# Kernel tuning notes

Hardware: AMD Instinct MI355X
Metric: run time of the kernel (lower is better)

Reference implementation:

```python
import jax, jax.numpy as jnp
import numpy as np

_USER_BASIS = [(0, 1), (2, 1), (4, 1), (8, 1), (1, 1), (6, 1), (10, 1), (12, 1),
               (3, -1), (5, -1), (9, -1), (14, 1), (7, 1), (11, 1), (13, 1), (15, -1)]
_MASK_TO_IDX = {mask: idx for idx, (mask, _) in enumerate(_USER_BASIS)}


def _blade_sign_pga(mask_a, mask_b):
    sign = 1
    for bit in range(4):
        if mask_a >> bit & 1:
            lower = mask_b & ((1 << bit) - 1)
            if bin(lower).count('1') % 2 == 1:
                sign = -sign
    return sign


def _build_pga_cayley_table():
    # table[k, i, j] = coeff of basis_k in basis_i * basis_j; values in {-1,0,+1}
    table = np.zeros((16, 16, 16), dtype=np.float32)
    for i, (mask_i, sign_i) in enumerate(_USER_BASIS):
        for j, (mask_j, sign_j) in enumerate(_USER_BASIS):
            if mask_i & mask_j & 1:  # shared null e0 -> product vanishes
                continue
            result_mask = mask_i ^ mask_j
            anticomm = _blade_sign_pga(mask_i, mask_j)
            k = _MASK_TO_IDX[result_mask]
            _, sign_k = _USER_BASIS[k]
            table[k, i, j] = float(sign_i * sign_j * anticomm * sign_k)
    return table


def setup_inputs() -> dict:
    key = jax.random.key(0)
    k1, k2 = jax.random.split(key)
    shape = (4, 4096, 128, 16)
    mv_a = jax.random.normal(k1, shape, dtype=jnp.float32)
    mv_b = jax.random.normal(k2, shape, dtype=jnp.float32)
    cayley = jnp.asarray(_build_pga_cayley_table())  # (16,16,16) buffer
    return {"mv_a": mv_a, "mv_b": mv_b, "cayley": cayley}


def reference(mv_a, mv_b, cayley):
    # Geometric product C[..., k] = sum_ij A[..., i] B[..., j] cayley[k, i, j]
    return jnp.einsum('...i,...j,kij->...k', mv_a, mv_b, cayley)
```

## Files before the change

### kernel.cpp

```cpp
#include <hip/hip_runtime.h>


namespace {

typedef float f32x4 __attribute__((ext_vector_type(4)));

struct CayleyLUT {
    int idx[16][16];
    int sgn[16][16];
};

constexpr CayleyLUT make_lut() {
    CayleyLUT L{};
    constexpr int MASK[16] = {0, 2, 4, 8, 1, 6, 10, 12, 3, 5, 9, 14, 7, 11, 13, 15};
    constexpr int SIGN[16] = {1, 1, 1, 1, 1, 1, 1, 1, -1, -1, -1, 1, 1, 1, 1, -1};
    for (int i = 0; i < 16; ++i) {
        for (int j = 0; j < 16; ++j) {
            L.idx[i][j] = 0;
            L.sgn[i][j] = 0;
            if (MASK[i] & MASK[j] & 1) continue;
            const int rm = MASK[i] ^ MASK[j];
            int k = 0;
            for (int t = 0; t < 16; ++t)
                if (MASK[t] == rm) k = t;
            int s = 1;
            for (int bit = 0; bit < 4; ++bit) {
                if ((MASK[i] >> bit) & 1) {
                    int lower = MASK[j] & ((1 << bit) - 1);
                    int c = 0;
                    for (int x = lower; x; x >>= 1) c += x & 1;
                    if (c & 1) s = -s;
                }
            }
            L.idx[i][j] = k;
            L.sgn[i][j] = SIGN[i] * SIGN[j] * s * SIGN[k];
        }
    }
    return L;
}

constexpr CayleyLUT LUT = make_lut();

__device__ __forceinline__ int slot(int m, int q) {
    return m * 16 + ((q ^ ((m >> 1) & 3)) << 2);
}

__device__ __forceinline__ void gp_compute(const float* a, const float* b, float* c) {
#pragma unroll
    for (int k = 0; k < 16; ++k) c[k] = 0.0f;
#pragma unroll
    for (int i = 0; i < 16; ++i) {
#pragma unroll
        for (int j = 0; j < 16; ++j) {
            const int s = LUT.sgn[i][j];
            if (s != 0) {
                const int k = LUT.idx[i][j];
                c[k] = fmaf(s > 0 ? a[i] : -a[i], b[j], c[k]);
            }
        }
    }
}

__global__ __launch_bounds__(256) void gp_kernel(const float* __restrict__ A,
                                                 const float* __restrict__ B,
                                                 float* __restrict__ C,
                                                 long long n_mv) {
    __shared__ float sA[256 * 16];
    __shared__ float sB[256 * 16];
    const int t = threadIdx.x;
    const long long base_mv = (long long)blockIdx.x * 256;
    const bool full = (base_mv + 256 <= n_mv);
    const int mv_here = full ? 256 : (int)(n_mv - base_mv);
    const int nf4 = mv_here * 4;

    const f32x4* __restrict__ A4 = reinterpret_cast<const f32x4*>(A) + base_mv * 4;
    const f32x4* __restrict__ B4 = reinterpret_cast<const f32x4*>(B) + base_mv * 4;
    f32x4* __restrict__ C4 = reinterpret_cast<f32x4*>(C) + base_mv * 4;

    if (full) {
#pragma unroll
        for (int r = 0; r < 4; ++r) {
            const int f = t + 256 * r;
            const f32x4 va = A4[f];
            const f32x4 vb = B4[f];
            const int o = slot(f >> 2, f & 3);
            *reinterpret_cast<f32x4*>(&sA[o]) = va;
            *reinterpret_cast<f32x4*>(&sB[o]) = vb;
        }
    } else {
#pragma unroll
        for (int r = 0; r < 4; ++r) {
            const int f = t + 256 * r;
            if (f < nf4) {
                const f32x4 va = A4[f];
                const f32x4 vb = B4[f];
                const int o = slot(f >> 2, f & 3);
                *reinterpret_cast<f32x4*>(&sA[o]) = va;
                *reinterpret_cast<f32x4*>(&sB[o]) = vb;
            }
        }
    }
    __syncthreads();

    if (full || t < mv_here) {
        float a[16], b[16];
#pragma unroll
        for (int q = 0; q < 4; ++q) {
            const int o = slot(t, q);
            const f32x4 va = *reinterpret_cast<const f32x4*>(&sA[o]);
            const f32x4 vb = *reinterpret_cast<const f32x4*>(&sB[o]);
            a[4 * q + 0] = va.x; a[4 * q + 1] = va.y; a[4 * q + 2] = va.z; a[4 * q + 3] = va.w;
            b[4 * q + 0] = vb.x; b[4 * q + 1] = vb.y; b[4 * q + 2] = vb.z; b[4 * q + 3] = vb.w;
        }
        float c[16];
        gp_compute(a, b, c);
#pragma unroll
        for (int q = 0; q < 4; ++q) {
            f32x4 v;
            v.x = c[4 * q + 0]; v.y = c[4 * q + 1]; v.z = c[4 * q + 2]; v.w = c[4 * q + 3];
            *reinterpret_cast<f32x4*>(&sA[slot(t, q)]) = v;
        }
    }
    __syncthreads();

    if (full) {
#pragma unroll
        for (int r = 0; r < 4; ++r) {
            const int f = t + 256 * r;
            const f32x4 v = *reinterpret_cast<const f32x4*>(&sA[slot(f >> 2, f & 3)]);
            __builtin_nontemporal_store(v, &C4[f]);
        }
    } else {
#pragma unroll
        for (int r = 0; r < 4; ++r) {
            const int f = t + 256 * r;
            if (f < nf4) {
                const f32x4 v = *reinterpret_cast<const f32x4*>(&sA[slot(f >> 2, f & 3)]);
                __builtin_nontemporal_store(v, &C4[f]);
            }
        }
    }
}

}

extern "C" void kernel_launch(void* const* d_in, const int* in_sizes, int n_in,
                              void* d_out, int out_size, void* d_ws, size_t ws_size,
                              hipStream_t stream) {
    const float* A = (const float*)d_in[0];
    const float* B = (const float*)d_in[1];
    float* C = (float*)d_out;
    const long long n_mv = (long long)in_sizes[0] / 16;
    const int nblocks = (int)((n_mv + 255) / 256);
    gp_kernel<<<nblocks, 256, 0, stream>>>(A, B, C, n_mv);
}
```

Before: 62.18 us.

## Replace LDS output staging with DPP quad transpose before coalesced stores

Each thread now computes a multivector chosen so that the four lanes of a quad together hold the four consecutive multivectors needed for one 64-lane coalesced store row. Results are exchanged inside each quad through DPP cross-lane moves instead of being written back to shared memory and read again. This removes the second __syncthreads and the LDS round trip for the output. The shared-memory swizzle is also changed to match the new read pattern. The cost is extra selects and DPP instructions, and the partial-block path now runs compute for every thread.

```diff
diff --git a/kernel.cpp b/kernel.cpp
--- a/kernel.cpp
+++ b/kernel.cpp
@@ -42,7 +42,33 @@
 constexpr CayleyLUT LUT = make_lut();
 
 __device__ __forceinline__ int slot(int m, int q) {
-    return m * 16 + ((q ^ ((m >> 1) & 3)) << 2);
+    return m * 16 + ((q ^ ((m >> 4) & 3)) << 2);
+}
+
+template <int CTRL>
+__device__ __forceinline__ float dppf(float x) {
+    return __int_as_float(
+        __builtin_amdgcn_update_dpp(0, __float_as_int(x), CTRL, 0xF, 0xF, true));
+}
+
+__device__ __forceinline__ void qtr(float& x0, float& x1, float& x2, float& x3,
+                                    bool l0, bool l1) {
+    const float s01 = l0 ? x0 : x1;
+    const float s23 = l0 ? x2 : x3;
+    const float r01 = dppf<0xB1>(s01);
+    const float r23 = dppf<0xB1>(s23);
+    const float m0 = l0 ? r01 : x0;
+    const float m1 = l0 ? x1 : r01;
+    const float m2 = l0 ? r23 : x2;
+    const float m3 = l0 ? x3 : r23;
+    const float s02 = l1 ? m0 : m2;
+    const float s13 = l1 ? m1 : m3;
+    const float r02 = dppf<0x4E>(s02);
+    const float r13 = dppf<0x4E>(s13);
+    x0 = l1 ? r02 : m0;
+    x2 = l1 ? m2 : r02;
+    x1 = l1 ? r13 : m1;
+    x3 = l1 ? m3 : r13;
 }
 
 __device__ __forceinline__ void gp_compute(const float* a, const float* b, float* c) {
@@ -68,6 +94,8 @@
     __shared__ float sA[256 * 16];
     __shared__ float sB[256 * 16];
     const int t = threadIdx.x;
+    const int w = t >> 6;
+    const int lane = t & 63;
     const long long base_mv = (long long)blockIdx.x * 256;
     const bool full = (base_mv + 256 <= n_mv);
     const int mv_here = full ? 256 : (int)(n_mv - base_mv);
@@ -102,40 +130,43 @@
     }
     __syncthreads();
 
-    if (full || t < mv_here) {
-        float a[16], b[16];
+    const int m = (w << 6) + ((lane & 3) << 4) + (lane >> 2);
+    float a[16], b[16];
 #pragma unroll
-        for (int q = 0; q < 4; ++q) {
-            const int o = slot(t, q);
-            const f32x4 va = *reinterpret_cast<const f32x4*>(&sA[o]);
-            const f32x4 vb = *reinterpret_cast<const f32x4*>(&sB[o]);
-            a[4 * q + 0] = va.x; a[4 * q + 1] = va.y; a[4 * q + 2] = va.z; a[4 * q + 3] = va.w;
-            b[4 * q + 0] = vb.x; b[4 * q + 1] = vb.y; b[4 * q + 2] = vb.z; b[4 * q + 3] = vb.w;
-        }
-        float c[16];
-        gp_compute(a, b, c);
+    for (int q = 0; q < 4; ++q) {
+        const f32x4 va = *reinterpret_cast<const f32x4*>(&sA[slot(m, q)]);
+        const f32x4 vb = *reinterpret_cast<const f32x4*>(&sB[slot(m, q)]);
 #pragma unroll
-        for (int q = 0; q < 4; ++q) {
-            f32x4 v;
-            v.x = c[4 * q + 0]; v.y = c[4 * q + 1]; v.z = c[4 * q + 2]; v.w = c[4 * q + 3];
-            *reinterpret_cast<f32x4*>(&sA[slot(t, q)]) = v;
+        for (int x = 0; x < 4; ++x) {
+            a[4 * q + x] = va[x];
+            b[4 * q + x] = vb[x];
         }
     }
-    __syncthreads();
+    float c[16];
+    gp_compute(a, b, c);
 
+    const bool l0 = (lane & 1) != 0;
+    const bool l1 = (lane & 2) != 0;
+#pragma unroll
+    for (int x = 0; x < 4; ++x) {
+        qtr(c[x], c[4 + x], c[8 + x], c[12 + x], l0, l1);
+    }
     if (full) {
 #pragma unroll
         for (int r = 0; r < 4; ++r) {
-            const int f = t + 256 * r;
-            const f32x4 v = *reinterpret_cast<const f32x4*>(&sA[slot(f >> 2, f & 3)]);
-            __builtin_nontemporal_store(v, &C4[f]);
+            f32x4 v;
+#pragma unroll
+            for (int x = 0; x < 4; ++x) v[x] = c[4 * r + x];
+            __builtin_nontemporal_store(v, &C4[(w << 8) + (r << 6) + lane]);
         }
     } else {
 #pragma unroll
         for (int r = 0; r < 4; ++r) {
-            const int f = t + 256 * r;
+            const int f = (w << 8) + (r << 6) + lane;
             if (f < nf4) {
-                const f32x4 v = *reinterpret_cast<const f32x4*>(&sA[slot(f >> 2, f & 3)]);
+                f32x4 v;
+#pragma unroll
+                for (int x = 0; x < 4; ++x) v[x] = c[4 * r + x];
                 __builtin_nontemporal_store(v, &C4[f]);
             }
         }
```

New measurement: 62.66 us. No clear change (+0.8%).
